# Kernel tuning notes

Measured on AMD Instinct MI355X. Metric: run time of the kernel, lower is better.

## Reference

```python
import jax, jax.numpy as jnp
import numpy as np

BN_EPS = 1e-3  # keras BatchNormalization default epsilon

@jax.custom_vjp
def ste_sign(x):
    # larq ste_sign: sign(x) with sign(0) -> +1
    return jnp.where(x >= 0, 1.0, -1.0).astype(x.dtype)

def _ste_fwd(x):
    return ste_sign(x), x

def _ste_bwd(x, g):
    # straight-through estimator, gradient clipped to |x| <= 1
    return (g * (jnp.abs(x) <= 1).astype(g.dtype),)

ste_sign.defvjp(_ste_fwd, _ste_bwd)

def setup_inputs() -> dict:
    key = jax.random.key(0)
    k1, k2, k3, k4, k5, k6 = jax.random.split(key, 6)
    B, D_IN, D_H = 32768, 2048, 512
    return {
        "input_tensor": jax.random.normal(k1, (B, D_IN), dtype=jnp.float32),
        "W": jax.random.normal(k2, (D_IN, D_H), dtype=jnp.float32) * 0.05,
        "b": jax.random.normal(k3, (D_H,), dtype=jnp.float32) * 0.01,
        "beta": jax.random.normal(k4, (D_H,), dtype=jnp.float32) * 0.01,
        "moving_mean": jax.random.normal(k5, (D_H,), dtype=jnp.float32) * 0.1,
        "moving_var": jax.random.uniform(k6, (D_H,), dtype=jnp.float32, minval=0.5, maxval=1.5),
    }

def reference(input_tensor, W, b, beta, moving_mean, moving_var):
    # QuantDense: binarize input and kernel, float GEMM over {-1,+1} values
    xq = ste_sign(input_tensor)                # [B, D_in]
    wq = ste_sign(W)                           # [D_in, D_h]
    y = jnp.matmul(xq, wq) + b                 # [B, D_h]
    # BatchNorm inference (training=False), scale=False (no gamma), center=True
    inv = jax.lax.rsqrt(moving_var + BN_EPS)
    return (y - moving_mean) * inv + beta
```

## Files before the change

kernel.cpp:

```cpp
#include <hip/hip_runtime.h>
#include <stdint.h>

#define D_IN 2048
#define D_H  512
#define BM   64
#define NST  16

typedef __attribute__((ext_vector_type(4)))  int i32x4;
typedef __attribute__((ext_vector_type(16))) int i32x16;

__device__ __forceinline__ void barrier_lgkm_only() {
  asm volatile("s_waitcnt lgkmcnt(0)" ::: "memory");
  __builtin_amdgcn_sched_barrier(0);
  __builtin_amdgcn_s_barrier();
  __builtin_amdgcn_sched_barrier(0);
}

__global__ __launch_bounds__(1024) void pack_wt_kernel(
    const float* __restrict__ W, char* __restrict__ Wf) {
  const int s = blockIdx.x;
  const int t = threadIdx.x >> 6;
  const int l = threadIdx.x & 63;
  const int n = t * 32 + (l & 31);
  const int kbase = s * 32 + 16 * (l >> 5);
  uint wq[4];
#pragma unroll
  for (int q = 0; q < 4; ++q) {
    uint w = 0x01010101u;
#pragma unroll
    for (int j = 0; j < 4; ++j) {
      uint bits = __float_as_uint(W[(size_t)(kbase + 4 * q + j) * D_H + n]);
      w ^= ((uint)((int)bits >> 31)) & (0xFEu << (8 * j));
    }
    wq[q] = w;
  }
  *(uint4*)(Wf + ((size_t)(s * 16 + t) * 64 + l) * 16) =
      make_uint4(wq[0], wq[1], wq[2], wq[3]);
}

__device__ __forceinline__ uint pack4(float4 v) {
  uint w = 0x01010101u;
  w ^= ((uint)((int)__float_as_uint(v.x) >> 31)) & 0x000000FEu;
  w ^= ((uint)((int)__float_as_uint(v.y) >> 31)) & 0x0000FE00u;
  w ^= ((uint)((int)__float_as_uint(v.z) >> 31)) & 0x00FE0000u;
  w ^= ((uint)((int)__float_as_uint(v.w) >> 31)) & 0xFE000000u;
  return w;
}

__global__ __launch_bounds__(512) void bgemm_kernel(
    const float* __restrict__ X, const char* __restrict__ Wf,
    const float* __restrict__ b, const float* __restrict__ beta,
    const float* __restrict__ mm, const float* __restrict__ mv,
    float* __restrict__ out) {
  __shared__ __align__(16) char XpL[2][8192];

  const int tid = threadIdx.x;
  const int l   = tid & 63;
  const int wv  = tid >> 6;
  const int am  = l & 31;
  const int ah  = l >> 5;
  const size_t m0 = (size_t)blockIdx.x * BM;
  const int colbase = wv * 64;

  const int r0 = tid >> 5;
  const int kw = tid & 31;
  const float* Xt = X + (m0 + r0) * D_IN + kw * 4;

  const int ws0 = r0 * 128 + (((kw >> 2) ^ (r0 & 7)) << 4) + (kw & 3) * 4;

  const int arow0 = am * 128;
  const int arow1 = arow0 + 32 * 128;
  const int akey  = am & 7;

  const char* Bb0 = Wf + (size_t)(2 * wv) * 1024 + (size_t)l * 16;
  const char* Bb1 = Bb0 + 1024;

  i32x16 acc00, acc01, acc10, acc11;
#pragma unroll
  for (int r = 0; r < 16; ++r) { acc00[r] = 0; acc01[r] = 0; acc10[r] = 0; acc11[r] = 0; }

  float4 vxa, vxb, vxc, vxd;

  vxa = *(const float4*)(Xt);
  vxb = *(const float4*)(Xt + 16 * D_IN);
  vxc = *(const float4*)(Xt + 32 * D_IN);
  vxd = *(const float4*)(Xt + 48 * D_IN);
  *(uint*)(XpL[0] + ws0)        = pack4(vxa);
  *(uint*)(XpL[0] + ws0 + 2048) = pack4(vxb);
  *(uint*)(XpL[0] + ws0 + 4096) = pack4(vxc);
  *(uint*)(XpL[0] + ws0 + 6144) = pack4(vxd);
  barrier_lgkm_only();

#pragma unroll 1
  for (int st = 0; st < NST; ++st) {
    const char* buf = &XpL[st & 1][0];
    const size_t so = (size_t)st * 65536;

    i32x4 B0a = *(const i32x4*)(Bb0 + so + 0 * 16384);
    i32x4 B0b = *(const i32x4*)(Bb1 + so + 0 * 16384);
    i32x4 B1a = *(const i32x4*)(Bb0 + so + 1 * 16384);
    i32x4 B1b = *(const i32x4*)(Bb1 + so + 1 * 16384);
    i32x4 B2a = *(const i32x4*)(Bb0 + so + 2 * 16384);
    i32x4 B2b = *(const i32x4*)(Bb1 + so + 2 * 16384);
    i32x4 B3a = *(const i32x4*)(Bb0 + so + 3 * 16384);
    i32x4 B3b = *(const i32x4*)(Bb1 + so + 3 * 16384);

    if (st + 1 < NST) {
      const float* xp = Xt + (st + 1) * 128;
      vxa = *(const float4*)(xp);
      vxb = *(const float4*)(xp + 16 * D_IN);
      vxc = *(const float4*)(xp + 32 * D_IN);
      vxd = *(const float4*)(xp + 48 * D_IN);
    }

    {
      i32x4 a0 = *(const i32x4*)(buf + arow0 + (((0 + ah) ^ akey) << 4));
      i32x4 a1 = *(const i32x4*)(buf + arow1 + (((0 + ah) ^ akey) << 4));
      acc00 = __builtin_amdgcn_mfma_i32_32x32x32_i8(a0, B0a, acc00, 0, 0, 0);
      acc10 = __builtin_amdgcn_mfma_i32_32x32x32_i8(a1, B0a, acc10, 0, 0, 0);
      acc01 = __builtin_amdgcn_mfma_i32_32x32x32_i8(a0, B0b, acc01, 0, 0, 0);
      acc11 = __builtin_amdgcn_mfma_i32_32x32x32_i8(a1, B0b, acc11, 0, 0, 0);
    }
    {
      i32x4 a0 = *(const i32x4*)(buf + arow0 + (((2 + ah) ^ akey) << 4));
      i32x4 a1 = *(const i32x4*)(buf + arow1 + (((2 + ah) ^ akey) << 4));
      acc00 = __builtin_amdgcn_mfma_i32_32x32x32_i8(a0, B1a, acc00, 0, 0, 0);
      acc10 = __builtin_amdgcn_mfma_i32_32x32x32_i8(a1, B1a, acc10, 0, 0, 0);
      acc01 = __builtin_amdgcn_mfma_i32_32x32x32_i8(a0, B1b, acc01, 0, 0, 0);
      acc11 = __builtin_amdgcn_mfma_i32_32x32x32_i8(a1, B1b, acc11, 0, 0, 0);
    }
    {
      i32x4 a0 = *(const i32x4*)(buf + arow0 + (((4 + ah) ^ akey) << 4));
      i32x4 a1 = *(const i32x4*)(buf + arow1 + (((4 + ah) ^ akey) << 4));
      acc00 = __builtin_amdgcn_mfma_i32_32x32x32_i8(a0, B2a, acc00, 0, 0, 0);
      acc10 = __builtin_amdgcn_mfma_i32_32x32x32_i8(a1, B2a, acc10, 0, 0, 0);
      acc01 = __builtin_amdgcn_mfma_i32_32x32x32_i8(a0, B2b, acc01, 0, 0, 0);
      acc11 = __builtin_amdgcn_mfma_i32_32x32x32_i8(a1, B2b, acc11, 0, 0, 0);
    }
    {
      i32x4 a0 = *(const i32x4*)(buf + arow0 + (((6 + ah) ^ akey) << 4));
      i32x4 a1 = *(const i32x4*)(buf + arow1 + (((6 + ah) ^ akey) << 4));
      acc00 = __builtin_amdgcn_mfma_i32_32x32x32_i8(a0, B3a, acc00, 0, 0, 0);
      acc10 = __builtin_amdgcn_mfma_i32_32x32x32_i8(a1, B3a, acc10, 0, 0, 0);
      acc01 = __builtin_amdgcn_mfma_i32_32x32x32_i8(a0, B3b, acc01, 0, 0, 0);
      acc11 = __builtin_amdgcn_mfma_i32_32x32x32_i8(a1, B3b, acc11, 0, 0, 0);
    }

    if (st + 1 < NST) {
      char* nbuf = &XpL[(st + 1) & 1][0];
      *(uint*)(nbuf + ws0)        = pack4(vxa);
      *(uint*)(nbuf + ws0 + 2048) = pack4(vxb);
      *(uint*)(nbuf + ws0 + 4096) = pack4(vxc);
      *(uint*)(nbuf + ws0 + 6144) = pack4(vxd);
    }
    barrier_lgkm_only();
  }

  const int rb = 4 * ah;
#pragma unroll
  for (int h = 0; h < 2; ++h) {
#pragma unroll
    for (int nt = 0; nt < 2; ++nt) {
      const i32x16 A = (h == 0) ? ((nt == 0) ? acc00 : acc01)
                                : ((nt == 0) ? acc10 : acc11);
      const int c = colbase + nt * 32 + am;
      const float bb  = b[c];
      const float mmc = mm[c];
      const float bec = beta[c];
      const float inv = rsqrtf(mv[c] + 1e-3f);
#pragma unroll
      for (int r = 0; r < 16; ++r) {
        const int row = (r & 3) + 8 * (r >> 2) + rb + 32 * h;
        out[(m0 + row) * D_H + c] = ((float)A[r] + bb - mmc) * inv + bec;
      }
    }
  }
}

extern "C" void kernel_launch(void* const* d_in, const int* in_sizes, int n_in,
                              void* d_out, int out_size, void* d_ws, size_t ws_size,
                              hipStream_t stream) {
  const float* X    = (const float*)d_in[0];
  const float* W    = (const float*)d_in[1];
  const float* b    = (const float*)d_in[2];
  const float* beta = (const float*)d_in[3];
  const float* mm   = (const float*)d_in[4];
  const float* mv   = (const float*)d_in[5];
  float* out = (float*)d_out;

  char* Wf = (char*)d_ws;

  pack_wt_kernel<<<dim3(D_IN / 32), dim3(1024), 0, stream>>>(W, Wf);

  const int M = in_sizes[0] / D_IN;
  bgemm_kernel<<<dim3(M / BM), dim3(512), 0, stream>>>(X, Wf, b, beta, mm, mv, out);
}
```

Before: 89.00 us.

## Split X binarization into bit-packed prepass and expand bits in GEMM kernel

Adds a separate kernel that packs sign bits of X into 64-bit ballot masks, and a new GEMM kernel that reads these bitmasks, expands them to int8 ±1 in registers, and feeds MFMA without LDS or barriers. The weight packing is permuted so its K order matches the bit layout, and the GEMM grid now splits the output columns across two blocks per row tile. The aim is to decouple the memory-bound X read from the MFMA loop and remove LDS traffic and synchronisation. The cost is an extra kernel launch, a workspace round trip for the packed X, and ALU work for bit expansion. The old fused path is kept as a fallback when the workspace is too small.

```diff
diff --git a/kernel.cpp b/kernel.cpp
--- a/kernel.cpp
+++ b/kernel.cpp
@@ -3,11 +3,161 @@
 
 #define D_IN 2048
 #define D_H  512
-#define BM   64
-#define NST  16
 
 typedef __attribute__((ext_vector_type(4)))  int i32x4;
 typedef __attribute__((ext_vector_type(16))) int i32x16;
+
+
+__global__ __launch_bounds__(1024) void pack_wt_perm_kernel(
+    const float* __restrict__ W, char* __restrict__ Wf) {
+  const int s = blockIdx.x;
+  const int t = threadIdx.x >> 6;
+  const int l = threadIdx.x & 63;
+  const int n  = t * 32 + (l & 31);
+  const int ah = l >> 5;
+  uint wq[4];
+#pragma unroll
+  for (int qd = 0; qd < 4; ++qd) {
+    uint w = 0x01010101u;
+#pragma unroll
+    for (int j = 0; j < 4; ++j) {
+      const int p = 4 * qd + j;
+      const int k = (s >> 3) * 256 + ((s & 1) * 32 + ah * 16 + p) * 4 + ((s >> 1) & 3);
+      uint bits = __float_as_uint(W[(size_t)k * D_H + n]);
+      w ^= ((uint)((int)bits >> 31)) & (0xFEu << (8 * j));
+    }
+    wq[qd] = w;
+  }
+  *(uint4*)(Wf + ((size_t)(s * 16 + t) * 64 + l) * 16) =
+      make_uint4(wq[0], wq[1], wq[2], wq[3]);
+}
+
+__global__ __launch_bounds__(256) void pack_x_kernel(
+    const float* __restrict__ X, unsigned long long* __restrict__ Xb) {
+  const int l  = threadIdx.x & 63;
+  const int wv = threadIdx.x >> 6;
+  const int mb = blockIdx.x >> 2;
+  const int r0 = (blockIdx.x & 3) * 16 + wv * 4;
+  unsigned long long* base = Xb + (size_t)mb * 2048;
+
+  for (int rr = 0; rr < 4; ++rr) {
+    const int r = r0 + rr;
+    const float4* Xr = (const float4*)(X + ((size_t)mb * 64 + r) * D_IN);
+#pragma unroll
+    for (int q = 0; q < 8; ++q) {
+      float4 v = Xr[q * 64 + l];
+      unsigned long long b0 = __ballot(v.x < 0.0f);
+      unsigned long long b1 = __ballot(v.y < 0.0f);
+      unsigned long long b2 = __ballot(v.z < 0.0f);
+      unsigned long long b3 = __ballot(v.w < 0.0f);
+      if (l == 0) {
+        base[q * 256 + 0 * 64 + r] = b0;
+        base[q * 256 + 1 * 64 + r] = b1;
+        base[q * 256 + 2 * 64 + r] = b2;
+        base[q * 256 + 3 * 64 + r] = b3;
+      }
+    }
+  }
+}
+
+__device__ __forceinline__ i32x4 expand16(uint m) {
+  i32x4 r;
+#pragma unroll
+  for (int j = 0; j < 4; ++j) {
+    uint bq = (m >> (4 * j)) & 0xFu;
+    uint spread = (bq * 0x00204081u) & 0x01010101u;
+    r[j] = (int)(0x01010101u | (spread * 0xFFu));
+  }
+  return r;
+}
+
+__global__ __launch_bounds__(512) void bgemm_bits_kernel(
+    const unsigned long long* __restrict__ Xb, const char* __restrict__ Wf,
+    const float* __restrict__ b, const float* __restrict__ beta,
+    const float* __restrict__ mm, const float* __restrict__ mv,
+    float* __restrict__ out) {
+  const int tid = threadIdx.x;
+  const int l   = tid & 63;
+  const int wv  = tid >> 6;
+  const int am  = l & 31;
+  const int ah  = l >> 5;
+  const int mb  = blockIdx.x >> 1;
+  const size_t m0 = (size_t)mb * 64;
+  const int colbase = (blockIdx.x & 1) * 256 + wv * 32;
+  const int tile = colbase >> 5;
+
+  const unsigned long long* xrow = Xb + (size_t)mb * 2048 + am;
+  const char* Bbase = Wf + (size_t)tile * 1024 + (size_t)l * 16;
+  const int sh0 = 16 * ah;
+  const int sh1 = 32 + 16 * ah;
+
+  i32x16 acc0, acc1;
+#pragma unroll
+  for (int r = 0; r < 16; ++r) { acc0[r] = 0; acc1[r] = 0; }
+
+  unsigned long long xa = xrow[0];
+  unsigned long long xb = xrow[32];
+  i32x4 B0 = *(const i32x4*)(Bbase);
+  i32x4 B1 = *(const i32x4*)(Bbase + 16384);
+  unsigned long long xa2, xb2;
+  i32x4 B2, B3;
+
+#pragma unroll 1
+  for (int sp = 0; sp < 32; sp += 2) {
+    {
+      const int spn = sp + 1;
+      const size_t xo = (size_t)(spn >> 2) * 256 + (size_t)(spn & 3) * 64;
+      xa2 = xrow[xo];
+      xb2 = xrow[xo + 32];
+      B2 = *(const i32x4*)(Bbase + (size_t)(2 * spn) * 16384);
+      B3 = *(const i32x4*)(Bbase + (size_t)(2 * spn + 1) * 16384);
+      i32x4 a;
+      a = expand16((uint)(xa >> sh0) & 0xFFFFu);
+      acc0 = __builtin_amdgcn_mfma_i32_32x32x32_i8(a, B0, acc0, 0, 0, 0);
+      a = expand16((uint)(xb >> sh0) & 0xFFFFu);
+      acc1 = __builtin_amdgcn_mfma_i32_32x32x32_i8(a, B0, acc1, 0, 0, 0);
+      a = expand16((uint)(xa >> sh1) & 0xFFFFu);
+      acc0 = __builtin_amdgcn_mfma_i32_32x32x32_i8(a, B1, acc0, 0, 0, 0);
+      a = expand16((uint)(xb >> sh1) & 0xFFFFu);
+      acc1 = __builtin_amdgcn_mfma_i32_32x32x32_i8(a, B1, acc1, 0, 0, 0);
+    }
+    {
+      const int spn = sp + 2;
+      if (spn < 32) {
+        const size_t xo = (size_t)(spn >> 2) * 256 + (size_t)(spn & 3) * 64;
+        xa = xrow[xo];
+        xb = xrow[xo + 32];
+        B0 = *(const i32x4*)(Bbase + (size_t)(2 * spn) * 16384);
+        B1 = *(const i32x4*)(Bbase + (size_t)(2 * spn + 1) * 16384);
+      }
+      i32x4 a;
+      a = expand16((uint)(xa2 >> sh0) & 0xFFFFu);
+      acc0 = __builtin_amdgcn_mfma_i32_32x32x32_i8(a, B2, acc0, 0, 0, 0);
+      a = expand16((uint)(xb2 >> sh0) & 0xFFFFu);
+      acc1 = __builtin_amdgcn_mfma_i32_32x32x32_i8(a, B2, acc1, 0, 0, 0);
+      a = expand16((uint)(xa2 >> sh1) & 0xFFFFu);
+      acc0 = __builtin_amdgcn_mfma_i32_32x32x32_i8(a, B3, acc0, 0, 0, 0);
+      a = expand16((uint)(xb2 >> sh1) & 0xFFFFu);
+      acc1 = __builtin_amdgcn_mfma_i32_32x32x32_i8(a, B3, acc1, 0, 0, 0);
+    }
+  }
+
+  const int rb = 4 * ah;
+  const int c  = colbase + am;
+  const float bb  = b[c];
+  const float mmc = mm[c];
+  const float bec = beta[c];
+  const float inv = rsqrtf(mv[c] + 1e-3f);
+#pragma unroll
+  for (int h = 0; h < 2; ++h) {
+    const i32x16 A = (h == 0) ? acc0 : acc1;
+#pragma unroll
+    for (int r = 0; r < 16; ++r) {
+      const int row = (r & 3) + 8 * (r >> 2) + rb + 32 * h;
+      out[(m0 + row) * D_H + c] = ((float)A[r] + bb - mmc) * inv + bec;
+    }
+  }
+}
 
 __device__ __forceinline__ void barrier_lgkm_only() {
   asm volatile("s_waitcnt lgkmcnt(0)" ::: "memory");
@@ -16,7 +166,7 @@
   __builtin_amdgcn_sched_barrier(0);
 }
 
-__global__ __launch_bounds__(1024) void pack_wt_kernel(
+__global__ __launch_bounds__(1024) void pack_wt_lin_kernel(
     const float* __restrict__ W, char* __restrict__ Wf) {
   const int s = blockIdx.x;
   const int t = threadIdx.x >> 6;
@@ -47,40 +197,33 @@
   return w;
 }
 
-__global__ __launch_bounds__(512) void bgemm_kernel(
+__global__ __launch_bounds__(512) void bgemm_fused_kernel(
     const float* __restrict__ X, const char* __restrict__ Wf,
     const float* __restrict__ b, const float* __restrict__ beta,
     const float* __restrict__ mm, const float* __restrict__ mv,
     float* __restrict__ out) {
   __shared__ __align__(16) char XpL[2][8192];
-
   const int tid = threadIdx.x;
   const int l   = tid & 63;
   const int wv  = tid >> 6;
   const int am  = l & 31;
   const int ah  = l >> 5;
-  const size_t m0 = (size_t)blockIdx.x * BM;
+  const size_t m0 = (size_t)blockIdx.x * 64;
   const int colbase = wv * 64;
-
   const int r0 = tid >> 5;
   const int kw = tid & 31;
   const float* Xt = X + (m0 + r0) * D_IN + kw * 4;
-
   const int ws0 = r0 * 128 + (((kw >> 2) ^ (r0 & 7)) << 4) + (kw & 3) * 4;
-
   const int arow0 = am * 128;
   const int arow1 = arow0 + 32 * 128;
   const int akey  = am & 7;
-
   const char* Bb0 = Wf + (size_t)(2 * wv) * 1024 + (size_t)l * 16;
   const char* Bb1 = Bb0 + 1024;
 
   i32x16 acc00, acc01, acc10, acc11;
 #pragma unroll
   for (int r = 0; r < 16; ++r) { acc00[r] = 0; acc01[r] = 0; acc10[r] = 0; acc11[r] = 0; }
-
   float4 vxa, vxb, vxc, vxd;
-
   vxa = *(const float4*)(Xt);
   vxb = *(const float4*)(Xt + 16 * D_IN);
   vxc = *(const float4*)(Xt + 32 * D_IN);
@@ -92,10 +235,9 @@
   barrier_lgkm_only();
 
 #pragma unroll 1
-  for (int st = 0; st < NST; ++st) {
+  for (int st = 0; st < 16; ++st) {
     const char* buf = &XpL[st & 1][0];
     const size_t so = (size_t)st * 65536;
-
     i32x4 B0a = *(const i32x4*)(Bb0 + so + 0 * 16384);
     i32x4 B0b = *(const i32x4*)(Bb1 + so + 0 * 16384);
     i32x4 B1a = *(const i32x4*)(Bb0 + so + 1 * 16384);
@@ -104,15 +246,13 @@
     i32x4 B2b = *(const i32x4*)(Bb1 + so + 2 * 16384);
     i32x4 B3a = *(const i32x4*)(Bb0 + so + 3 * 16384);
     i32x4 B3b = *(const i32x4*)(Bb1 + so + 3 * 16384);
-
-    if (st + 1 < NST) {
+    if (st + 1 < 16) {
       const float* xp = Xt + (st + 1) * 128;
       vxa = *(const float4*)(xp);
       vxb = *(const float4*)(xp + 16 * D_IN);
       vxc = *(const float4*)(xp + 32 * D_IN);
       vxd = *(const float4*)(xp + 48 * D_IN);
     }
-
     {
       i32x4 a0 = *(const i32x4*)(buf + arow0 + (((0 + ah) ^ akey) << 4));
       i32x4 a1 = *(const i32x4*)(buf + arow1 + (((0 + ah) ^ akey) << 4));
@@ -145,8 +285,7 @@
       acc01 = __builtin_amdgcn_mfma_i32_32x32x32_i8(a0, B3b, acc01, 0, 0, 0);
       acc11 = __builtin_amdgcn_mfma_i32_32x32x32_i8(a1, B3b, acc11, 0, 0, 0);
     }
-
-    if (st + 1 < NST) {
+    if (st + 1 < 16) {
       char* nbuf = &XpL[(st + 1) & 1][0];
       *(uint*)(nbuf + ws0)        = pack4(vxa);
       *(uint*)(nbuf + ws0 + 2048) = pack4(vxb);
@@ -188,10 +327,19 @@
   const float* mv   = (const float*)d_in[5];
   float* out = (float*)d_out;
 
+  const int M = in_sizes[0] / D_IN;
   char* Wf = (char*)d_ws;
 
-  pack_wt_kernel<<<dim3(D_IN / 32), dim3(1024), 0, stream>>>(W, Wf);
-
-  const int M = in_sizes[0] / D_IN;
-  bgemm_kernel<<<dim3(M / BM), dim3(512), 0, stream>>>(X, Wf, b, beta, mm, mv, out);
-}
+  const size_t need = (1u << 20) + (size_t)(M / 64) * 16384;
+  if (ws_size >= need) {
+    unsigned long long* Xb = (unsigned long long*)(Wf + (1u << 20));
+    pack_wt_perm_kernel<<<dim3(64), dim3(1024), 0, stream>>>(W, Wf);
+    pack_x_kernel<<<dim3(M / 16), dim3(256), 0, stream>>>(X, Xb);
+    bgemm_bits_kernel<<<dim3(M / 32), dim3(512), 0, stream>>>(Xb, Wf, b, beta,
+                                                              mm, mv, out);
+  } else {
+    pack_wt_lin_kernel<<<dim3(64), dim3(1024), 0, stream>>>(W, Wf);
+    bgemm_fused_kernel<<<dim3(M / 64), dim3(512), 0, stream>>>(X, Wf, b, beta,
+                                                               mm, mv, out);
+  }
+}
```

Measured after the change: 128.4 us. 44.3% more time.
